# Performance work log

Hardware: AMD Instinct MI355X
Metric: run time of the kernel (lower is better)

## Reference

```python
import jax, jax.numpy as jnp
import numpy as np

N, B, E, H, L, NF = 32768, 2048, 524288, 128, 7, 10
NODE_F = 60  # 10 frames * (loc 3 + vel 3)
OUT_F = 30   # 10 frames * 3


def _mlp(x, W1, b1, W2, b2):
    return jax.nn.relu(x @ W1 + b1) @ W2 + b2


def _lin(key, fan_in, fan_out):
    s = 1.0 / np.sqrt(fan_in)
    kw, kb = jax.random.split(key)
    W = jax.random.uniform(kw, (fan_in, fan_out), jnp.float32, -s, s)
    b = jax.random.uniform(kb, (fan_out,), jnp.float32, -s, s)
    return W, b


def setup_inputs() -> dict:
    key = jax.random.key(0)
    ks = jax.random.split(key, 12)
    p = {}
    p["loc"] = jax.random.normal(ks[0], (N, NF, 3), jnp.float32)
    p["vel"] = jax.random.normal(ks[1], (N, NF, 3), jnp.float32)
    p["y"] = jax.random.normal(ks[2], (N, NF, 3), jnp.float32)
    p["edge_index"] = jax.random.randint(ks[3], (2, E), 0, N, dtype=jnp.int64)
    p["batch_size"] = B
    # embedder: Linear(60,H) -> ReLU -> Linear(H,H)
    p["emb_W1"], p["emb_b1"] = _lin(ks[4], NODE_F, H)
    p["emb_W2"], p["emb_b2"] = _lin(ks[5], H, H)
    # per-layer message net Linear(2H,H)->ReLU->Linear(H,H); update net Linear(2H,H)->ReLU->Linear(H,H)
    mW1, mb1, mW2, mb2, uW1, ub1, uW2, ub2 = [], [], [], [], [], [], [], []
    for i in range(L):
        k = jax.random.fold_in(ks[6], i)
        k1, k2, k3, k4 = jax.random.split(k, 4)
        a, b = _lin(k1, 2 * H, H); mW1.append(a); mb1.append(b)
        a, b = _lin(k2, H, H); mW2.append(a); mb2.append(b)
        a, b = _lin(k3, 2 * H, H); uW1.append(a); ub1.append(b)
        a, b = _lin(k4, H, H); uW2.append(a); ub2.append(b)
    p["msg_W1"] = jnp.stack(mW1); p["msg_b1"] = jnp.stack(mb1)
    p["msg_W2"] = jnp.stack(mW2); p["msg_b2"] = jnp.stack(mb2)
    p["upd_W1"] = jnp.stack(uW1); p["upd_b1"] = jnp.stack(ub1)
    p["upd_W2"] = jnp.stack(uW2); p["upd_b2"] = jnp.stack(ub2)
    # head: Linear(H,H) -> ReLU -> Linear(H,30)
    p["head_W1"], p["head_b1"] = _lin(ks[7], H, H)
    p["head_W2"], p["head_b2"] = _lin(ks[8], H, OUT_F)
    return p


def reference(loc, vel, y, edge_index, batch_size,
              emb_W1, emb_b1, emb_W2, emb_b2,
              msg_W1, msg_b1, msg_W2, msg_b2,
              upd_W1, upd_b1, upd_W2, upd_b2,
              head_W1, head_b1, head_W2, head_b2):
    n = loc.shape[0]
    src, dst = edge_index[0], edge_index[1]  # x_j = x[src], x_i = x[dst] (PyG source_to_target)
    x = jnp.concatenate([loc, vel], axis=-1).reshape(n, -1)  # (N, 60)
    x = _mlp(x, emb_W1, emb_b1, emb_W2, emb_b2)              # (N, H)
    for i in range(L):
        m_in = jnp.concatenate([x[dst], x[src]], axis=-1)    # (E, 2H) cat(x_i, x_j)
        msg = _mlp(m_in, msg_W1[i], msg_b1[i], msg_W2[i], msg_b2[i])  # (E, H)
        agg = jax.ops.segment_sum(msg, dst, num_segments=n)  # scatter-add at targets
        x = _mlp(jnp.concatenate([x, agg], axis=-1), upd_W1[i], upd_b1[i], upd_W2[i], upd_b2[i])
    x = _mlp(x, head_W1, head_b1, head_W2, head_b2)          # (N, 30)
    loc_pred = x.reshape(n, NF, 3) + loc
    d = jnp.sqrt(jnp.sum((loc_pred - y) ** 2, axis=-1))      # (N, NF)
    ade_loss = d.reshape(batch_size, -1, NF).mean(axis=-1).mean(axis=-1)  # (B,)
    fde = jnp.sqrt(jnp.sum((loc_pred[:, -1, :] - y[:, -1, :]) ** 2, axis=-1))  # (N,)
    fde_loss = fde.reshape(batch_size, -1).mean(axis=-1)     # (B,)
    backprop_loss = ade_loss.mean()
    return backprop_loss, ade_loss, fde_loss
```

## Files before the change

### kernel.cpp

```cpp
#include <hip/hip_runtime.h>
#include <hip/hip_bf16.h>
#include <stdint.h>

#define HH 128

typedef __attribute__((ext_vector_type(8))) short short8;
typedef __attribute__((ext_vector_type(4))) float floatx4;

typedef __attribute__((address_space(3))) uint32_t lds_u32_t;
typedef const __attribute__((address_space(1))) uint32_t gbl_u32_t;

__device__ __forceinline__ void gl_lds16(const void* g, void* l) {
  __builtin_amdgcn_global_load_lds((gbl_u32_t*)g, (lds_u32_t*)l, 16, 0, 0);
}

__device__ __forceinline__ float bf2f(short v) {
  union { uint32_t u; float f; } x; x.u = ((uint32_t)(uint16_t)v) << 16; return x.f;
}
__device__ __forceinline__ short f2bf(float f) {
  union { float f; uint32_t u; } x; x.f = f;
  uint32_t r = x.u + 0x7fffu + ((x.u >> 16) & 1u);
  return (short)(r >> 16);
}
__device__ __forceinline__ float rdf(const void* p, int i, int fl) {
  return fl ? bf2f(((const short*)p)[i]) : ((const float*)p)[i];
}


__global__ void detect_zero(const int* __restrict__ eidx, int* iflag, int* dflag,
                            int* __restrict__ counts, float* accp,
                            const uint32_t* __restrict__ loc, int N) {
  int g = blockIdx.x * 256 + threadIdx.x;
  if (g < N) counts[g] = 0;
  if (blockIdx.x == 0) {
    __shared__ int nz, cnt;
    if (threadIdx.x == 0) { nz = 0; cnt = 0; *accp = 0.f; }
    __syncthreads();
    int any = 0;
    for (int i = threadIdx.x; i < 1024; i += 256) any |= (eidx[2 * i + 1] != 0);
    if (any) atomicOr(&nz, 1);
    uint32_t u = loc[threadIdx.x];
    int e = (u >> 7) & 0xFF;
    if (e >= 100 && e <= 140) atomicAdd(&cnt, 1);
    __syncthreads();
    if (threadIdx.x == 0) {
      *iflag = (nz == 0) ? 1 : 0;
      *dflag = (cnt >= 192) ? 1 : 0;
    }
  }
}


__global__ void pad_input(const void* __restrict__ loc, const void* __restrict__ vel,
                          short* __restrict__ dst, const int* __restrict__ dflag) {
  int fl = *dflag;
  int idx = blockIdx.x * 256 + threadIdx.x;
  int j = idx & 63, i = idx >> 6;
  short v = 0;
  if (j < 60) {
    int f = j / 6, c = j % 6;
    float x = (c < 3) ? rdf(loc, (i * 10 + f) * 3 + c, fl)
                      : rdf(vel, (i * 10 + f) * 3 + (c - 3), fl);
    v = f2bf(x);
  }
  dst[idx] = v;
}

struct WPrep {
  const void* src[8];
  unsigned long long dstoff[8];
  int L[8], K[8], Nn[8], Kp[8], Np[8];
  int bstart[9];
};

__global__ void prep_w(WPrep a, short* __restrict__ wbase, const int* __restrict__ dflag) {
  int fl = *dflag;
  int b = blockIdx.x;
  int s = 0;
  while (b >= a.bstart[s + 1]) ++s;
  int idx = (b - a.bstart[s]) * 256 + threadIdx.x;
  int Kp = a.Kp[s], Np = a.Np[s], K = a.K[s], Nn = a.Nn[s];
  int tot = a.L[s] * Np * Kp;
  if (idx >= tot) return;
  int k = idx % Kp; int rest = idx / Kp; int n = rest % Np; int l = rest / Np;
  short v = 0;
  if (k < K && n < Nn) v = f2bf(rdf(a.src[s], (l * K + k) * Nn + n, fl));
  wbase[a.dstoff[s] + idx] = v;
}

struct BPrep {
  const void* src[8];
  int n[8];
  int estart[9];
};

__global__ void prep_b(BPrep a, float* __restrict__ bias, const int* __restrict__ dflag) {
  int fl = *dflag;
  int idx = blockIdx.x * 256 + threadIdx.x;
  if (idx >= a.estart[8]) return;
  int s = 0;
  while (idx >= a.estart[s + 1]) ++s;
  int j = idx - a.estart[s];
  bias[idx] = (j < a.n[s]) ? rdf(a.src[s], j, fl) : 0.0f;
}


__global__ void fold_kernel(const short* __restrict__ updW1T, const short* __restrict__ msgW2T,
                            short* __restrict__ updW1Tf, const float* __restrict__ msgB2f,
                            float* __restrict__ b2U) {
  if (blockIdx.x < 896) {
    int idx = blockIdx.x * 256 + threadIdx.x;
    int k = idx & 255; int n = (idx >> 8) & 127; int l = idx >> 15;
    if (k < 128) { updW1Tf[idx] = updW1T[idx]; return; }
    int kk = k - 128;
    const short* w2 = msgW2T + l * 128 * 128;
    const short* u1 = updW1T + l * 128 * 256 + n * 256 + 128;
    float s = 0.f;
    for (int j = 0; j < 128; ++j) s += bf2f(w2[j * 128 + kk]) * bf2f(u1[j]);
    updW1Tf[idx] = f2bf(s);
  } else {
    int idx = (blockIdx.x - 896) * 256 + threadIdx.x;
    if (idx >= 7 * 128) return;
    int n = idx & 127, l = idx >> 7;
    const short* u1 = updW1T + l * 128 * 256 + n * 256 + 128;
    const float* b2 = msgB2f + l * 128;
    float s = 0.f;
    for (int j = 0; j < 128; ++j) s += b2[j] * bf2f(u1[j]);
    b2U[idx] = s;
  }
}


__global__ void hist_kernel(const int* __restrict__ eidx, const int* __restrict__ iflag,
                            int* __restrict__ counts, int E) {
  int e = blockIdx.x * 256 + threadIdx.x;
  if (e >= E) return;
  int fl = *iflag;
  int d = fl ? eidx[2 * (E + e)] : eidx[E + e];
  atomicAdd(&counts[d], 1);
}

__global__ void scan_bsum(const int* __restrict__ counts, int* __restrict__ bsums, int N) {
  int i = blockIdx.x * 256 + threadIdx.x;
  int v = (i < N) ? counts[i] : 0;
#pragma unroll
  for (int off = 1; off < 64; off <<= 1) v += __shfl_xor(v, off);
  __shared__ int ws4[4];
  if ((threadIdx.x & 63) == 0) ws4[threadIdx.x >> 6] = v;
  __syncthreads();
  if (threadIdx.x == 0) bsums[blockIdx.x] = ws4[0] + ws4[1] + ws4[2] + ws4[3];
}

__global__ void scan_final(const int* __restrict__ counts, const int* __restrict__ bsums,
                           int* __restrict__ row_start, int* __restrict__ cursor,
                           float* __restrict__ deg, int N, int E) {
  int t = threadIdx.x;
  __shared__ int shb[2];
  __shared__ int wsum[4];
  int v = (t < 128 && t < (int)blockIdx.x) ? bsums[t] : 0;
#pragma unroll
  for (int off = 1; off < 64; off <<= 1) v += __shfl_xor(v, off);
  if (t == 0) shb[0] = v;
  if (t == 64) shb[1] = v;
  int i = blockIdx.x * 256 + t;
  int c = (i < N) ? counts[i] : 0;
  int lane = t & 63, w = t >> 6;
  int x = c;
#pragma unroll
  for (int off = 1; off < 64; off <<= 1) {
    int u = __shfl_up(x, off);
    if (lane >= off) x += u;
  }
  if (lane == 63) wsum[w] = x;
  __syncthreads();
  int wpre = 0;
#pragma unroll
  for (int k = 0; k < 4; ++k)
    if (k < w) wpre += wsum[k];
  int excl = shb[0] + shb[1] + wpre + x - c;
  if (i < N) {
    row_start[i] = excl;
    cursor[i] = excl;
    deg[i] = (float)c;
  }
  if (i == N - 1) row_start[N] = E;
}

__global__ void scatter_kernel(const int* __restrict__ eidx, const int* __restrict__ iflag,
                               int* __restrict__ cursor, int* __restrict__ ssrc, int E) {
  int e = blockIdx.x * 256 + threadIdx.x;
  if (e >= E) return;
  int fl = *iflag;
  int d = fl ? eidx[2 * (E + e)] : eidx[E + e];
  int sv = fl ? eidx[2 * e] : eidx[e];
  int pos = atomicAdd(&cursor[d], 1);
  ssrc[pos] = sv;
}


__global__ __launch_bounds__(256)
void edge_agg(const uint32_t* __restrict__ Pp, const uint32_t* __restrict__ Qp,
              const int* __restrict__ ssrc, const int* __restrict__ row_start,
              uint32_t* __restrict__ Hagg, int Ntot) {
  int w = threadIdx.x >> 6, lane = threadIdx.x & 63;
  int d = blockIdx.x * 4 + w;
  if (d >= Ntot) return;
  uint32_t pv = Pp[(size_t)d * 64 + lane];
  float px = bf2f((short)(pv & 0xffff));
  float py = bf2f((short)(pv >> 16));
  int s0 = row_start[d], s1 = row_start[d + 1];
  float ax = 0.f, ay = 0.f;
  int e = s0;
  for (; e + 8 <= s1; e += 8) {
    int idx[8]; uint32_t q[8];
#pragma unroll
    for (int u = 0; u < 8; ++u) idx[u] = ssrc[e + u];
#pragma unroll
    for (int u = 0; u < 8; ++u) q[u] = Qp[(size_t)idx[u] * 64 + lane];
#pragma unroll
    for (int u = 0; u < 8; ++u) {
      float hx = px + bf2f((short)(q[u] & 0xffff));
      float hy = py + bf2f((short)(q[u] >> 16));
      ax += hx > 0.f ? hx : 0.f;
      ay += hy > 0.f ? hy : 0.f;
    }
  }
  if (e + 4 <= s1) {
    int idx[4]; uint32_t q[4];
#pragma unroll
    for (int u = 0; u < 4; ++u) idx[u] = ssrc[e + u];
#pragma unroll
    for (int u = 0; u < 4; ++u) q[u] = Qp[(size_t)idx[u] * 64 + lane];
#pragma unroll
    for (int u = 0; u < 4; ++u) {
      float hx = px + bf2f((short)(q[u] & 0xffff));
      float hy = py + bf2f((short)(q[u] >> 16));
      ax += hx > 0.f ? hx : 0.f;
      ay += hy > 0.f ? hy : 0.f;
    }
    e += 4;
  }
  if (e + 2 <= s1) {
    int i0 = ssrc[e], i1 = ssrc[e + 1];
    uint32_t q0 = Qp[(size_t)i0 * 64 + lane];
    uint32_t q1 = Qp[(size_t)i1 * 64 + lane];
    float hx = px + bf2f((short)(q0 & 0xffff)), hy = py + bf2f((short)(q0 >> 16));
    ax += hx > 0.f ? hx : 0.f; ay += hy > 0.f ? hy : 0.f;
    hx = px + bf2f((short)(q1 & 0xffff)); hy = py + bf2f((short)(q1 >> 16));
    ax += hx > 0.f ? hx : 0.f; ay += hy > 0.f ? hy : 0.f;
    e += 2;
  }
  if (e < s1) {
    int i0 = ssrc[e];
    uint32_t q0 = Qp[(size_t)i0 * 64 + lane];
    float hx = px + bf2f((short)(q0 & 0xffff));
    float hy = py + bf2f((short)(q0 >> 16));
    ax += hx > 0.f ? hx : 0.f;
    ay += hy > 0.f ? hy : 0.f;
  }
  uint32_t packed = (uint32_t)(uint16_t)f2bf(ax) | ((uint32_t)(uint16_t)f2bf(ay) << 16);
  Hagg[(size_t)d * 64 + lane] = packed;
}


__device__ __forceinline__ void write_aslots32(char* lds, const floatx4 v[2][4],
                                               int wc, int quad, int l16) {
#pragma unroll
  for (int mt = 0; mt < 2; ++mt)
#pragma unroll
    for (int nt = 0; nt < 4; ++nt) {
      int s2 = wc * 2 + (nt >> 1);
      int qc = (nt & 1) * 2 + (l16 >> 3);
      char* base = lds + (size_t)(s2 * 2 + mt) * 1024 + 2 * (l16 & 7);
#pragma unroll
      for (int r = 0; r < 4; ++r)
        *(short*)(base + (quad * 4 + r + 16 * qc) * 16) = f2bf(v[mt][nt][r]);
    }
}

template <int NT, int TS>
__device__ __forceinline__ void gemm32(const char* lds, int wc, floatx4 acc[2][NT], int lane) {
  const char* ldsB = lds + 8192;
#pragma unroll
  for (int s2 = 0; s2 < 4; ++s2) {
    short8 af[2];
#pragma unroll
    for (int mt = 0; mt < 2; ++mt)
      af[mt] = *(const short8*)(lds + (s2 * 2 + mt) * 1024 + lane * 16);
    short8 bf[NT];
#pragma unroll
    for (int nt = 0; nt < NT; ++nt)
      bf[nt] = *(const short8*)(ldsB + (s2 * TS + wc * NT + nt) * 1024 + lane * 16);
#pragma unroll
    for (int mt = 0; mt < 2; ++mt)
#pragma unroll
      for (int nt = 0; nt < NT; ++nt)
        acc[mt][nt] = __builtin_amdgcn_mfma_f32_16x16x32_bf16(af[mt], bf[nt], acc[mt][nt], 0, 0, 0);
  }
}


template <int MODE>
__global__ __launch_bounds__(128, 2)
void mlp_fused(const short* __restrict__ Asrc, const short* __restrict__ Asrc2,
               const short* __restrict__ W1T, const float* __restrict__ b1,
               const short* __restrict__ W2T, const float* __restrict__ b2,
               const float* __restrict__ deg, const float* __restrict__ b2Uv,
               const short* __restrict__ pqW1, const float* __restrict__ pqB1,
               const short* __restrict__ pq2W, const float* __restrict__ pq2B,
               short* __restrict__ xout, short* __restrict__ Pout,
               short* __restrict__ Qout, float* __restrict__ out32) {
  constexpr int K1 = (MODE == 0) ? 64 : 256;
  constexpr int NSA = K1 / 32;
  constexpr int PQS = (MODE == 3) ? 128 : 256;

  __shared__ __align__(16) char lds[40960];
  char* ldsB = lds + 8192;

  const int tid = threadIdx.x;
  const int wc = tid >> 6, lane = tid & 63;
  const int quad = lane >> 4, l16 = lane & 15;
  const int R0 = blockIdx.x * 32;
  const int CB = wc * 64;

  if constexpr (MODE == 0) {
#pragma unroll
    for (int c = 0; c < 8; ++c) {
      int slot = wc * 8 + c;
      int s = slot >> 3, t = slot & 7;
      gl_lds16(W1T + (t * 16 + l16) * 64 + s * 32 + quad * 8,
               ldsB + slot * 1024 + lane * 16);
    }
  } else {
#pragma unroll
    for (int c = 0; c < 16; ++c) {
      int slot = wc * 16 + c;
      int s2 = slot >> 3, t = slot & 7;
      gl_lds16(W1T + (t * 16 + l16) * 256 + s2 * 32 + quad * 8,
               ldsB + slot * 1024 + lane * 16);
    }
  }

  short8 afrag[NSA][2];
  if constexpr (MODE == 0) {
#pragma unroll
    for (int mt = 0; mt < 2; ++mt) {
      int m = R0 + mt * 16 + l16;
      const short* pr = Asrc + (size_t)m * 64;
#pragma unroll
      for (int s = 0; s < 2; ++s) afrag[s][mt] = *(const short8*)(pr + s * 32 + quad * 8);
    }
  } else {
#pragma unroll
    for (int mt = 0; mt < 2; ++mt) {
      int m = R0 + mt * 16 + l16;
      const short* pr = Asrc + (size_t)m * HH;
      const short* ar = Asrc2 + (size_t)m * HH;
#pragma unroll
      for (int s = 0; s < 4; ++s) {
        afrag[s][mt] = *(const short8*)(pr + s * 32 + quad * 8);
        afrag[s + 4][mt] = *(const short8*)(ar + s * 32 + quad * 8);
      }
    }
  }

  float b1f[4], b2f[4], pb1[4], b2u[4];
  float dvals[2][4];
#pragma unroll
  for (int t = 0; t < 4; ++t) {
    int col = CB + t * 16 + l16;
    b1f[t] = b1[col];
    b2f[t] = b2[col];
    pb1[t] = pqB1[col];
  }
  if constexpr (MODE != 0) {
#pragma unroll
    for (int t = 0; t < 4; ++t) b2u[t] = b2Uv[CB + t * 16 + l16];
#pragma unroll
    for (int mt = 0; mt < 2; ++mt)
#pragma unroll
      for (int r = 0; r < 4; ++r)
        dvals[mt][r] = deg[R0 + mt * 16 + quad * 4 + r];
  }

  __syncthreads();

  floatx4 zero4 = {0.f, 0.f, 0.f, 0.f};
  floatx4 acc[2][4];
#pragma unroll
  for (int mt = 0; mt < 2; ++mt)
#pragma unroll
    for (int t = 0; t < 4; ++t) acc[mt][t] = zero4;
  {
    constexpr int NS0 = (MODE == 0) ? 2 : 4;
#pragma unroll
    for (int s = 0; s < NS0; ++s) {
      short8 bfrag[4];
#pragma unroll
      for (int nt = 0; nt < 4; ++nt)
        bfrag[nt] = *(const short8*)(ldsB + (s * 8 + wc * 4 + nt) * 1024 + lane * 16);
#pragma unroll
      for (int mt = 0; mt < 2; ++mt)
#pragma unroll
        for (int nt = 0; nt < 4; ++nt)
          acc[mt][nt] = __builtin_amdgcn_mfma_f32_16x16x32_bf16(afrag[s][mt], bfrag[nt], acc[mt][nt], 0, 0, 0);
    }
  }

  if constexpr (MODE != 0) {
    __syncthreads();
#pragma unroll
    for (int c = 0; c < 16; ++c) {
      int slot = wc * 16 + c;
      int s2 = slot >> 3, t = slot & 7;
      gl_lds16(W1T + (t * 16 + l16) * 256 + 128 + s2 * 32 + quad * 8,
               ldsB + slot * 1024 + lane * 16);
    }
    __syncthreads();
#pragma unroll
    for (int s = 0; s < 4; ++s) {
      short8 bfrag[4];
#pragma unroll
      for (int nt = 0; nt < 4; ++nt)
        bfrag[nt] = *(const short8*)(ldsB + (s * 8 + wc * 4 + nt) * 1024 + lane * 16);
#pragma unroll
      for (int mt = 0; mt < 2; ++mt)
#pragma unroll
        for (int nt = 0; nt < 4; ++nt)
          acc[mt][nt] = __builtin_amdgcn_mfma_f32_16x16x32_bf16(afrag[4 + s][mt], bfrag[nt], acc[mt][nt], 0, 0, 0);
    }
  }

  __syncthreads();

#pragma unroll
  for (int c = 0; c < 16; ++c) {
    int slot = wc * 16 + c;
    int s2 = slot >> 3, t = slot & 7;
    gl_lds16(W2T + (t * 16 + l16) * HH + s2 * 32 + quad * 8,
             ldsB + slot * 1024 + lane * 16);
  }
  {
    floatx4 hv[2][4];
#pragma unroll
    for (int mt = 0; mt < 2; ++mt)
#pragma unroll
      for (int nt = 0; nt < 4; ++nt)
#pragma unroll
        for (int r = 0; r < 4; ++r) {
          float h = acc[mt][nt][r] + b1f[nt];
          if constexpr (MODE != 0) h += dvals[mt][r] * b2u[nt];
          hv[mt][nt][r] = h > 0.f ? h : 0.f;
        }
    write_aslots32(lds, hv, wc, quad, l16);
  }

  __syncthreads();

  floatx4 acc2[2][4];
#pragma unroll
  for (int mt = 0; mt < 2; ++mt)
#pragma unroll
    for (int t = 0; t < 4; ++t) acc2[mt][t] = zero4;
  gemm32<4, 8>(lds, wc, acc2, lane);

  floatx4 xv[2][4];
#pragma unroll
  for (int mt = 0; mt < 2; ++mt)
#pragma unroll
    for (int nt = 0; nt < 4; ++nt)
#pragma unroll
      for (int r = 0; r < 4; ++r)
        xv[mt][nt][r] = acc2[mt][nt][r] + b2f[nt];

  if constexpr (MODE != 3) {
#pragma unroll
    for (int mt = 0; mt < 2; ++mt)
#pragma unroll
      for (int nt = 0; nt < 4; ++nt) {
        int col = CB + nt * 16 + l16;
#pragma unroll
        for (int r = 0; r < 4; ++r) {
          int row = R0 + mt * 16 + quad * 4 + r;
          xout[(size_t)row * HH + col] = f2bf(xv[mt][nt][r]);
        }
      }
  }

  __syncthreads();

  write_aslots32(lds, xv, wc, quad, l16);
#pragma unroll
  for (int c = 0; c < 16; ++c) {
    int slot = wc * 16 + c;
    int s2 = slot >> 3, t = slot & 7;
    gl_lds16(pqW1 + (t * 16 + l16) * PQS + s2 * 32 + quad * 8,
             ldsB + slot * 1024 + lane * 16);
  }

  __syncthreads();

  floatx4 accc[2][4];
#pragma unroll
  for (int mt = 0; mt < 2; ++mt)
#pragma unroll
    for (int t = 0; t < 4; ++t) accc[mt][t] = zero4;
  gemm32<4, 8>(lds, wc, accc, lane);

  if constexpr (MODE == 3) {
    floatx4 h2[2][4];
#pragma unroll
    for (int mt = 0; mt < 2; ++mt)
#pragma unroll
      for (int nt = 0; nt < 4; ++nt)
#pragma unroll
        for (int r = 0; r < 4; ++r) {
          float h = accc[mt][nt][r] + pb1[nt];
          h2[mt][nt][r] = h > 0.f ? h : 0.f;
        }
    __syncthreads();
    write_aslots32(lds, h2, wc, quad, l16);
#pragma unroll
    for (int c = 0; c < 4; ++c) {
      int slot = wc * 4 + c;
      int s2 = slot >> 1, t = slot & 1;
      gl_lds16(pq2W + (t * 16 + l16) * 128 + s2 * 32 + quad * 8,
               ldsB + slot * 1024 + lane * 16);
    }
    __syncthreads();
    floatx4 acco[2][1];
#pragma unroll
    for (int mt = 0; mt < 2; ++mt) acco[mt][0] = zero4;
    gemm32<1, 2>(lds, wc, acco, lane);
    float ob = pq2B[wc * 16 + l16];
#pragma unroll
    for (int mt = 0; mt < 2; ++mt) {
      int col = wc * 16 + l16;
#pragma unroll
      for (int r = 0; r < 4; ++r) {
        int row = R0 + mt * 16 + quad * 4 + r;
        out32[(size_t)row * 32 + col] = acco[mt][0][r] + ob;
      }
    }
  } else {
#pragma unroll
    for (int mt = 0; mt < 2; ++mt)
#pragma unroll
      for (int nt = 0; nt < 4; ++nt) {
        int col = CB + nt * 16 + l16;
#pragma unroll
        for (int r = 0; r < 4; ++r) {
          int row = R0 + mt * 16 + quad * 4 + r;
          Pout[(size_t)row * HH + col] = f2bf(accc[mt][nt][r] + pb1[nt]);
        }
      }
    __syncthreads();
#pragma unroll
    for (int c = 0; c < 16; ++c) {
      int slot = wc * 16 + c;
      int s2 = slot >> 3, t = slot & 7;
      gl_lds16(pqW1 + (t * 16 + l16) * 256 + 128 + s2 * 32 + quad * 8,
               ldsB + slot * 1024 + lane * 16);
    }
    __syncthreads();
    floatx4 accq[2][4];
#pragma unroll
    for (int mt = 0; mt < 2; ++mt)
#pragma unroll
      for (int t = 0; t < 4; ++t) accq[mt][t] = zero4;
    gemm32<4, 8>(lds, wc, accq, lane);
#pragma unroll
    for (int mt = 0; mt < 2; ++mt)
#pragma unroll
      for (int nt = 0; nt < 4; ++nt) {
        int col = CB + nt * 16 + l16;
#pragma unroll
        for (int r = 0; r < 4; ++r) {
          int row = R0 + mt * 16 + quad * 4 + r;
          Qout[(size_t)row * HH + col] = f2bf(accq[mt][nt][r]);
        }
      }
  }
}


__global__ void loss_kernel(const float* __restrict__ out32, const void* __restrict__ loc,
                            const void* __restrict__ yv, const int* __restrict__ dflag,
                            float* __restrict__ out, float* __restrict__ acc, int NB) {
  int fl = *dflag;
  int i = blockIdx.x * 256 + threadIdx.x;
  const float* o = out32 + (size_t)i * 32;
  float dsum = 0.f, fde = 0.f;
#pragma unroll
  for (int f = 0; f < 10; ++f) {
    float dx = o[f * 3 + 0] + rdf(loc, i * 30 + f * 3 + 0, fl) - rdf(yv, i * 30 + f * 3 + 0, fl);
    float dy = o[f * 3 + 1] + rdf(loc, i * 30 + f * 3 + 1, fl) - rdf(yv, i * 30 + f * 3 + 1, fl);
    float dz = o[f * 3 + 2] + rdf(loc, i * 30 + f * 3 + 2, fl) - rdf(yv, i * 30 + f * 3 + 2, fl);
    float d = sqrtf(dx * dx + dy * dy + dz * dz);
    dsum += d;
    if (f == 9) fde = d;
  }
#pragma unroll
  for (int m = 1; m < 16; m <<= 1) {
    dsum += __shfl_xor(dsum, m);
    fde += __shfl_xor(fde, m);
  }
  if ((threadIdx.x & 15) == 0) {
    int b = i >> 4;
    out[1 + b] = dsum / 160.0f;
    out[1 + NB + b] = fde / 16.0f;
    unsafeAtomicAdd(acc, dsum);
  }
}

__global__ void final_kernel(const float* __restrict__ acc, float* __restrict__ out, float inv) {
  if (threadIdx.x == 0) out[0] = *acc * inv;
}


extern "C" void kernel_launch(void* const* d_in, const int* in_sizes, int n_in,
                              void* d_out, int out_size, void* d_ws, size_t ws_size,
                              hipStream_t stream) {
  const void* loc = d_in[0];
  const void* vel = d_in[1];
  const void* yv = d_in[2];
  const int* eidx = (const int*)d_in[3];

  const int N = in_sizes[0] / 30;
  const int E = in_sizes[3] / 2;
  const int L = 7;
  const int NB = N / 16;

  const size_t MB = 1024 * 1024;
  char* ws = (char*)d_ws;
  short* x = (short*)ws;
  short* P = (short*)(ws + 8 * MB);
  short* Qs = (short*)(ws + 24 * MB);
  short* Hagg = (short*)(ws + 32 * MB);
  short* updW1Tf = (short*)(ws + 40 * MB);
  int* bsums = (int*)(ws + 41 * MB);
  short* wbase = (short*)(ws + 48 * MB);
  const unsigned long long OFF_EMBW1 = 0;
  const unsigned long long OFF_EMBW2 = 8192;
  const unsigned long long OFF_HEADW1 = 24576;
  const unsigned long long OFF_HEADW2 = 40960;
  const unsigned long long OFF_MSGW1 = 45056;
  const unsigned long long OFF_MSGW2 = 274432;
  const unsigned long long OFF_UPDW1 = 389120;
  const unsigned long long OFF_UPDW2 = 618496;
  short* embW1T = wbase + OFF_EMBW1;
  short* embW2T = wbase + OFF_EMBW2;
  short* headW1T = wbase + OFF_HEADW1;
  short* headW2T = wbase + OFF_HEADW2;
  short* msgW1T = wbase + OFF_MSGW1;
  short* msgW2T = wbase + OFF_MSGW2;
  short* updW1T = wbase + OFF_UPDW1;
  short* updW2T = wbase + OFF_UPDW2;
  float* bias = (float*)(ws + 49 * MB + 512 * 1024);
  float* embB1f = bias;
  float* embB2f = bias + 128;
  float* msgB1f = bias + 256;
  float* msgB2f = bias + 1152;
  float* updB1f = bias + 2048;
  float* updB2f = bias + 2944;
  float* headB1f = bias + 3840;
  float* headB2f = bias + 3968;
  float* b2U = bias + 4096;
  int* counts = (int*)(ws + 49 * MB + 768 * 1024);
  int* row_start = (int*)(ws + 50 * MB);
  int* cursor = (int*)(ws + 50 * MB + 256 * 1024);
  float* deg = (float*)(ws + 50 * MB + 512 * 1024);
  int* iflag = (int*)(ws + 50 * MB + 768 * 1024);
  int* dflag = iflag + 16;
  float* accp = (float*)(iflag + 32);
  int* ssrc = (int*)(ws + 51 * MB);
  short* in64 = (short*)(ws + 53 * MB);
  float* out32 = (float*)(ws + 57 * MB);

  const int NBLK = (N + 255) / 256;

  detect_zero<<<NBLK, 256, 0, stream>>>(eidx, iflag, dflag, counts, accp,
                                        (const uint32_t*)loc, N);
  hist_kernel<<<(E + 255) / 256, 256, 0, stream>>>(eidx, iflag, counts, E);
  scan_bsum<<<NBLK, 256, 0, stream>>>(counts, bsums, N);
  scan_final<<<NBLK, 256, 0, stream>>>(counts, bsums, row_start, cursor, deg, N, E);
  scatter_kernel<<<(E + 255) / 256, 256, 0, stream>>>(eidx, iflag, cursor, ssrc, E);

  pad_input<<<(N * 64) / 256, 256, 0, stream>>>(loc, vel, in64, dflag);

  {
    WPrep a;
    const void* srcs[8] = {d_in[5], d_in[7], d_in[17], d_in[19],
                           d_in[9], d_in[11], d_in[13], d_in[15]};
    unsigned long long offs[8] = {OFF_EMBW1, OFF_EMBW2, OFF_HEADW1, OFF_HEADW2,
                                  OFF_MSGW1, OFF_MSGW2, OFF_UPDW1, OFF_UPDW2};
    int Ls[8] = {1, 1, 1, 1, 7, 7, 7, 7};
    int Ks[8] = {60, 128, 128, 128, 256, 128, 256, 128};
    int Ns[8] = {128, 128, 128, 30, 128, 128, 128, 128};
    int Kps[8] = {64, 128, 128, 128, 256, 128, 256, 128};
    int Nps[8] = {128, 128, 128, 32, 128, 128, 128, 128};
    int cum = 0;
    for (int s = 0; s < 8; ++s) {
      a.src[s] = srcs[s]; a.dstoff[s] = offs[s];
      a.L[s] = Ls[s]; a.K[s] = Ks[s]; a.Nn[s] = Ns[s]; a.Kp[s] = Kps[s]; a.Np[s] = Nps[s];
      a.bstart[s] = cum;
      cum += (Ls[s] * Nps[s] * Kps[s] + 255) / 256;
    }
    a.bstart[8] = cum;
    prep_w<<<cum, 256, 0, stream>>>(a, wbase, dflag);
  }
  {
    BPrep a;
    const void* srcs[8] = {d_in[6], d_in[8], d_in[10], d_in[12],
                           d_in[14], d_in[16], d_in[18], d_in[20]};
    int ns[8] = {128, 128, 896, 896, 896, 896, 128, 30};
    int es[9] = {0, 128, 256, 1152, 2048, 2944, 3840, 3968, 4000};
    for (int s = 0; s < 8; ++s) { a.src[s] = srcs[s]; a.n[s] = ns[s]; a.estart[s] = es[s]; }
    a.estart[8] = es[8];
    prep_b<<<16, 256, 0, stream>>>(a, bias, dflag);
  }

  fold_kernel<<<900, 256, 0, stream>>>(updW1T, msgW2T, updW1Tf, msgB2f, b2U);

  mlp_fused<0><<<N / 32, 128, 0, stream>>>(in64, nullptr,
      embW1T, embB1f, embW2T, embB2f, nullptr, nullptr,
      msgW1T, msgB1f, nullptr, nullptr, x, P, Qs, nullptr);

  for (int l = 0; l < L; ++l) {
    edge_agg<<<(N + 3) / 4, 256, 0, stream>>>((const uint32_t*)P, (const uint32_t*)Qs,
                                              ssrc, row_start, (uint32_t*)Hagg, N);
    if (l < L - 1) {
      mlp_fused<2><<<N / 32, 128, 0, stream>>>(x, Hagg,
          updW1Tf + l * 128 * 256, updB1f + l * 128, updW2T + l * 128 * 128, updB2f + l * 128,
          deg, b2U + l * 128,
          msgW1T + (l + 1) * 128 * 256, msgB1f + (l + 1) * 128, nullptr, nullptr,
          x, P, Qs, nullptr);
    } else {
      mlp_fused<3><<<N / 32, 128, 0, stream>>>(x, Hagg,
          updW1Tf + l * 128 * 256, updB1f + l * 128, updW2T + l * 128 * 128, updB2f + l * 128,
          deg, b2U + l * 128,
          headW1T, headB1f, headW2T, headB2f,
          nullptr, nullptr, nullptr, out32);
    }
  }

  loss_kernel<<<N / 256, 256, 0, stream>>>(out32, loc, yv, dflag, (float*)d_out, accp, NB);
  final_kernel<<<1, 64, 0, stream>>>(accp, (float*)d_out, 1.0f / 327680.0f);
}
```

Before: 567.8 us.

## Double mlp_fused row tile to 64 with 4 waves; fold final kernel into loss

The fused MLP kernel now processes 64 rows per block with four waves arranged 2x2 (row and column halves), so each weight tile staged in LDS is reused across twice as many rows. The full 256-wide first-layer weight is loaded at once into a 64 KB LDS buffer, which removes the second load-and-sync phase. The separate final kernel is replaced by a last-block ticket inside the loss kernel, saving one launch. The cost is more LDS per block, which may limit occupancy, and half as many blocks in the grid.

```diff
diff --git a/kernel.cpp b/kernel.cpp
--- a/kernel.cpp
+++ b/kernel.cpp
@@ -28,13 +28,13 @@
 
 
 __global__ void detect_zero(const int* __restrict__ eidx, int* iflag, int* dflag,
-                            int* __restrict__ counts, float* accp,
+                            int* __restrict__ counts, float* accp, int* ticket,
                             const uint32_t* __restrict__ loc, int N) {
   int g = blockIdx.x * 256 + threadIdx.x;
   if (g < N) counts[g] = 0;
   if (blockIdx.x == 0) {
     __shared__ int nz, cnt;
-    if (threadIdx.x == 0) { nz = 0; cnt = 0; *accp = 0.f; }
+    if (threadIdx.x == 0) { nz = 0; cnt = 0; *accp = 0.f; *ticket = 0; }
     __syncthreads();
     int any = 0;
     for (int i = threadIdx.x; i < 1024; i += 256) any |= (eidx[2 * i + 1] != 0);
@@ -263,30 +263,33 @@
 }
 
 
-__device__ __forceinline__ void write_aslots32(char* lds, const floatx4 v[2][4],
-                                               int wc, int quad, int l16) {
-#pragma unroll
-  for (int mt = 0; mt < 2; ++mt)
+__device__ __forceinline__ void write_aslots64(char* lds, const floatx4 v[2][4],
+                                               int wr, int wc, int quad, int l16) {
+#pragma unroll
+  for (int mt = 0; mt < 2; ++mt) {
+    int g = wr * 2 + mt;
 #pragma unroll
     for (int nt = 0; nt < 4; ++nt) {
       int s2 = wc * 2 + (nt >> 1);
       int qc = (nt & 1) * 2 + (l16 >> 3);
-      char* base = lds + (size_t)(s2 * 2 + mt) * 1024 + 2 * (l16 & 7);
+      char* base = lds + (size_t)(s2 * 4 + g) * 1024 + 2 * (l16 & 7);
 #pragma unroll
       for (int r = 0; r < 4; ++r)
         *(short*)(base + (quad * 4 + r + 16 * qc) * 16) = f2bf(v[mt][nt][r]);
     }
+  }
 }
 
 template <int NT, int TS>
-__device__ __forceinline__ void gemm32(const char* lds, int wc, floatx4 acc[2][NT], int lane) {
-  const char* ldsB = lds + 8192;
+__device__ __forceinline__ void gemm64(const char* lds, int wr, int wc,
+                                       floatx4 acc[2][NT], int lane) {
+  const char* ldsB = lds + 16384;
 #pragma unroll
   for (int s2 = 0; s2 < 4; ++s2) {
     short8 af[2];
 #pragma unroll
     for (int mt = 0; mt < 2; ++mt)
-      af[mt] = *(const short8*)(lds + (s2 * 2 + mt) * 1024 + lane * 16);
+      af[mt] = *(const short8*)(lds + (s2 * 4 + wr * 2 + mt) * 1024 + lane * 16);
     short8 bf[NT];
 #pragma unroll
     for (int nt = 0; nt < NT; ++nt)
@@ -301,7 +304,7 @@
 
 
 template <int MODE>
-__global__ __launch_bounds__(128, 2)
+__global__ __launch_bounds__(256, 2)
 void mlp_fused(const short* __restrict__ Asrc, const short* __restrict__ Asrc2,
                const short* __restrict__ W1T, const float* __restrict__ b1,
                const short* __restrict__ W2T, const float* __restrict__ b2,
@@ -310,23 +313,23 @@
                const short* __restrict__ pq2W, const float* __restrict__ pq2B,
                short* __restrict__ xout, short* __restrict__ Pout,
                short* __restrict__ Qout, float* __restrict__ out32) {
-  constexpr int K1 = (MODE == 0) ? 64 : 256;
-  constexpr int NSA = K1 / 32;
+  constexpr int NSA = (MODE == 0) ? 2 : 8;
   constexpr int PQS = (MODE == 3) ? 128 : 256;
 
-  __shared__ __align__(16) char lds[40960];
-  char* ldsB = lds + 8192;
+  __shared__ __align__(16) char lds[65536];
+  char* ldsB = lds + 16384;
 
   const int tid = threadIdx.x;
-  const int wc = tid >> 6, lane = tid & 63;
+  const int w = tid >> 6, lane = tid & 63;
   const int quad = lane >> 4, l16 = lane & 15;
-  const int R0 = blockIdx.x * 32;
+  const int wr = w >> 1, wc = w & 1;
+  const int R0 = blockIdx.x * 64;
   const int CB = wc * 64;
 
   if constexpr (MODE == 0) {
 #pragma unroll
-    for (int c = 0; c < 8; ++c) {
-      int slot = wc * 8 + c;
+    for (int c = 0; c < 4; ++c) {
+      int slot = w * 4 + c;
       int s = slot >> 3, t = slot & 7;
       gl_lds16(W1T + (t * 16 + l16) * 64 + s * 32 + quad * 8,
                ldsB + slot * 1024 + lane * 16);
@@ -334,10 +337,10 @@
   } else {
 #pragma unroll
     for (int c = 0; c < 16; ++c) {
-      int slot = wc * 16 + c;
-      int s2 = slot >> 3, t = slot & 7;
-      gl_lds16(W1T + (t * 16 + l16) * 256 + s2 * 32 + quad * 8,
-               ldsB + slot * 1024 + lane * 16);
+      int slot = w * 16 + c;
+      int s = slot >> 3, t = slot & 7;
+      gl_lds16(W1T + (t * 16 + l16) * 256 + s * 32 + quad * 8,
+               lds + slot * 1024 + lane * 16);
     }
   }
 
@@ -345,7 +348,7 @@
   if constexpr (MODE == 0) {
 #pragma unroll
     for (int mt = 0; mt < 2; ++mt) {
-      int m = R0 + mt * 16 + l16;
+      int m = R0 + wr * 32 + mt * 16 + l16;
       const short* pr = Asrc + (size_t)m * 64;
 #pragma unroll
       for (int s = 0; s < 2; ++s) afrag[s][mt] = *(const short8*)(pr + s * 32 + quad * 8);
@@ -353,7 +356,7 @@
   } else {
 #pragma unroll
     for (int mt = 0; mt < 2; ++mt) {
-      int m = R0 + mt * 16 + l16;
+      int m = R0 + wr * 32 + mt * 16 + l16;
       const short* pr = Asrc + (size_t)m * HH;
       const short* ar = Asrc2 + (size_t)m * HH;
 #pragma unroll
@@ -380,7 +383,7 @@
     for (int mt = 0; mt < 2; ++mt)
 #pragma unroll
       for (int r = 0; r < 4; ++r)
-        dvals[mt][r] = deg[R0 + mt * 16 + quad * 4 + r];
+        dvals[mt][r] = deg[R0 + wr * 32 + mt * 16 + quad * 4 + r];
   }
 
   __syncthreads();
@@ -391,10 +394,9 @@
   for (int mt = 0; mt < 2; ++mt)
 #pragma unroll
     for (int t = 0; t < 4; ++t) acc[mt][t] = zero4;
-  {
-    constexpr int NS0 = (MODE == 0) ? 2 : 4;
-#pragma unroll
-    for (int s = 0; s < NS0; ++s) {
+  if constexpr (MODE == 0) {
+#pragma unroll
+    for (int s = 0; s < 2; ++s) {
       short8 bfrag[4];
 #pragma unroll
       for (int nt = 0; nt < 4; ++nt)
@@ -405,37 +407,26 @@
         for (int nt = 0; nt < 4; ++nt)
           acc[mt][nt] = __builtin_amdgcn_mfma_f32_16x16x32_bf16(afrag[s][mt], bfrag[nt], acc[mt][nt], 0, 0, 0);
     }
-  }
-
-  if constexpr (MODE != 0) {
-    __syncthreads();
-#pragma unroll
-    for (int c = 0; c < 16; ++c) {
-      int slot = wc * 16 + c;
-      int s2 = slot >> 3, t = slot & 7;
-      gl_lds16(W1T + (t * 16 + l16) * 256 + 128 + s2 * 32 + quad * 8,
-               ldsB + slot * 1024 + lane * 16);
-    }
-    __syncthreads();
-#pragma unroll
-    for (int s = 0; s < 4; ++s) {
+  } else {
+#pragma unroll
+    for (int s = 0; s < 8; ++s) {
       short8 bfrag[4];
 #pragma unroll
       for (int nt = 0; nt < 4; ++nt)
-        bfrag[nt] = *(const short8*)(ldsB + (s * 8 + wc * 4 + nt) * 1024 + lane * 16);
+        bfrag[nt] = *(const short8*)(lds + (s * 8 + wc * 4 + nt) * 1024 + lane * 16);
 #pragma unroll
       for (int mt = 0; mt < 2; ++mt)
 #pragma unroll
         for (int nt = 0; nt < 4; ++nt)
-          acc[mt][nt] = __builtin_amdgcn_mfma_f32_16x16x32_bf16(afrag[4 + s][mt], bfrag[nt], acc[mt][nt], 0, 0, 0);
+          acc[mt][nt] = __builtin_amdgcn_mfma_f32_16x16x32_bf16(afrag[s][mt], bfrag[nt], acc[mt][nt], 0, 0, 0);
     }
   }
 
   __syncthreads();
 
 #pragma unroll
-  for (int c = 0; c < 16; ++c) {
-    int slot = wc * 16 + c;
+  for (int c = 0; c < 8; ++c) {
+    int slot = w * 8 + c;
     int s2 = slot >> 3, t = slot & 7;
     gl_lds16(W2T + (t * 16 + l16) * HH + s2 * 32 + quad * 8,
              ldsB + slot * 1024 + lane * 16);
@@ -452,7 +443,7 @@
           if constexpr (MODE != 0) h += dvals[mt][r] * b2u[nt];
           hv[mt][nt][r] = h > 0.f ? h : 0.f;
         }
-    write_aslots32(lds, hv, wc, quad, l16);
+    write_aslots64(lds, hv, wr, wc, quad, l16);
   }
 
   __syncthreads();
@@ -462,7 +453,7 @@
   for (int mt = 0; mt < 2; ++mt)
 #pragma unroll
     for (int t = 0; t < 4; ++t) acc2[mt][t] = zero4;
-  gemm32<4, 8>(lds, wc, acc2, lane);
+  gemm64<4, 8>(lds, wr, wc, acc2, lane);
 
   floatx4 xv[2][4];
 #pragma unroll
@@ -481,7 +472,7 @@
         int col = CB + nt * 16 + l16;
 #pragma unroll
         for (int r = 0; r < 4; ++r) {
-          int row = R0 + mt * 16 + quad * 4 + r;
+          int row = R0 + wr * 32 + mt * 16 + quad * 4 + r;
           xout[(size_t)row * HH + col] = f2bf(xv[mt][nt][r]);
         }
       }
@@ -489,10 +480,10 @@
 
   __syncthreads();
 
-  write_aslots32(lds, xv, wc, quad, l16);
-#pragma unroll
-  for (int c = 0; c < 16; ++c) {
-    int slot = wc * 16 + c;
+  write_aslots64(lds, xv, wr, wc, quad, l16);
+#pragma unroll
+  for (int c = 0; c < 8; ++c) {
+    int slot = w * 8 + c;
     int s2 = slot >> 3, t = slot & 7;
     gl_lds16(pqW1 + (t * 16 + l16) * PQS + s2 * 32 + quad * 8,
              ldsB + slot * 1024 + lane * 16);
@@ -505,7 +496,7 @@
   for (int mt = 0; mt < 2; ++mt)
 #pragma unroll
     for (int t = 0; t < 4; ++t) accc[mt][t] = zero4;
-  gemm32<4, 8>(lds, wc, accc, lane);
+  gemm64<4, 8>(lds, wr, wc, accc, lane);
 
   if constexpr (MODE == 3) {
     floatx4 h2[2][4];
@@ -519,10 +510,10 @@
           h2[mt][nt][r] = h > 0.f ? h : 0.f;
         }
     __syncthreads();
-    write_aslots32(lds, h2, wc, quad, l16);
-#pragma unroll
-    for (int c = 0; c < 4; ++c) {
-      int slot = wc * 4 + c;
+    write_aslots64(lds, h2, wr, wc, quad, l16);
+#pragma unroll
+    for (int c = 0; c < 2; ++c) {
+      int slot = w * 2 + c;
       int s2 = slot >> 1, t = slot & 1;
       gl_lds16(pq2W + (t * 16 + l16) * 128 + s2 * 32 + quad * 8,
                ldsB + slot * 1024 + lane * 16);
@@ -531,14 +522,14 @@
     floatx4 acco[2][1];
 #pragma unroll
     for (int mt = 0; mt < 2; ++mt) acco[mt][0] = zero4;
-    gemm32<1, 2>(lds, wc, acco, lane);
+    gemm64<1, 2>(lds, wr, wc, acco, lane);
     float ob = pq2B[wc * 16 + l16];
 #pragma unroll
     for (int mt = 0; mt < 2; ++mt) {
       int col = wc * 16 + l16;
 #pragma unroll
       for (int r = 0; r < 4; ++r) {
-        int row = R0 + mt * 16 + quad * 4 + r;
+        int row = R0 + wr * 32 + mt * 16 + quad * 4 + r;
         out32[(size_t)row * 32 + col] = acco[mt][0][r] + ob;
       }
     }
@@ -550,14 +541,14 @@
         int col = CB + nt * 16 + l16;
 #pragma unroll
         for (int r = 0; r < 4; ++r) {
-          int row = R0 + mt * 16 + quad * 4 + r;
+          int row = R0 + wr * 32 + mt * 16 + quad * 4 + r;
           Pout[(size_t)row * HH + col] = f2bf(accc[mt][nt][r] + pb1[nt]);
         }
       }
     __syncthreads();
 #pragma unroll
-    for (int c = 0; c < 16; ++c) {
-      int slot = wc * 16 + c;
+    for (int c = 0; c < 8; ++c) {
+      int slot = w * 8 + c;
       int s2 = slot >> 3, t = slot & 7;
       gl_lds16(pqW1 + (t * 16 + l16) * 256 + 128 + s2 * 32 + quad * 8,
                ldsB + slot * 1024 + lane * 16);
@@ -568,7 +559,7 @@
     for (int mt = 0; mt < 2; ++mt)
 #pragma unroll
       for (int t = 0; t < 4; ++t) accq[mt][t] = zero4;
-    gemm32<4, 8>(lds, wc, accq, lane);
+    gemm64<4, 8>(lds, wr, wc, accq, lane);
 #pragma unroll
     for (int mt = 0; mt < 2; ++mt)
 #pragma unroll
@@ -576,7 +567,7 @@
         int col = CB + nt * 16 + l16;
 #pragma unroll
         for (int r = 0; r < 4; ++r) {
-          int row = R0 + mt * 16 + quad * 4 + r;
+          int row = R0 + wr * 32 + mt * 16 + quad * 4 + r;
           Qout[(size_t)row * HH + col] = f2bf(accq[mt][nt][r]);
         }
       }
@@ -586,7 +577,8 @@
 
 __global__ void loss_kernel(const float* __restrict__ out32, const void* __restrict__ loc,
                             const void* __restrict__ yv, const int* __restrict__ dflag,
-                            float* __restrict__ out, float* __restrict__ acc, int NB) {
+                            float* __restrict__ out, float* __restrict__ acc,
+                            int* __restrict__ ticket, int NB, int nblocks, float inv) {
   int fl = *dflag;
   int i = blockIdx.x * 256 + threadIdx.x;
   const float* o = out32 + (size_t)i * 32;
@@ -611,10 +603,15 @@
     out[1 + NB + b] = fde / 16.0f;
     unsafeAtomicAdd(acc, dsum);
   }
-}
-
-__global__ void final_kernel(const float* __restrict__ acc, float* __restrict__ out, float inv) {
-  if (threadIdx.x == 0) out[0] = *acc * inv;
+  __threadfence();
+  __syncthreads();
+  if (threadIdx.x == 0) {
+    int old = atomicAdd(ticket, 1);
+    if (old == nblocks - 1) {
+      float v = unsafeAtomicAdd(acc, 0.0f);
+      out[0] = v * inv;
+    }
+  }
 }
 
 
@@ -673,13 +670,14 @@
   int* iflag = (int*)(ws + 50 * MB + 768 * 1024);
   int* dflag = iflag + 16;
   float* accp = (float*)(iflag + 32);
+  int* ticket = iflag + 48;
   int* ssrc = (int*)(ws + 51 * MB);
   short* in64 = (short*)(ws + 53 * MB);
   float* out32 = (float*)(ws + 57 * MB);
 
   const int NBLK = (N + 255) / 256;
 
-  detect_zero<<<NBLK, 256, 0, stream>>>(eidx, iflag, dflag, counts, accp,
+  detect_zero<<<NBLK, 256, 0, stream>>>(eidx, iflag, dflag, counts, accp, ticket,
                                         (const uint32_t*)loc, N);
   hist_kernel<<<(E + 255) / 256, 256, 0, stream>>>(eidx, iflag, counts, E);
   scan_bsum<<<NBLK, 256, 0, stream>>>(counts, bsums, N);
@@ -722,7 +720,7 @@
 
   fold_kernel<<<900, 256, 0, stream>>>(updW1T, msgW2T, updW1Tf, msgB2f, b2U);
 
-  mlp_fused<0><<<N / 32, 128, 0, stream>>>(in64, nullptr,
+  mlp_fused<0><<<N / 64, 256, 0, stream>>>(in64, nullptr,
       embW1T, embB1f, embW2T, embB2f, nullptr, nullptr,
       msgW1T, msgB1f, nullptr, nullptr, x, P, Qs, nullptr);
 
@@ -730,13 +728,13 @@
     edge_agg<<<(N + 3) / 4, 256, 0, stream>>>((const uint32_t*)P, (const uint32_t*)Qs,
                                               ssrc, row_start, (uint32_t*)Hagg, N);
     if (l < L - 1) {
-      mlp_fused<2><<<N / 32, 128, 0, stream>>>(x, Hagg,
+      mlp_fused<2><<<N / 64, 256, 0, stream>>>(x, Hagg,
           updW1Tf + l * 128 * 256, updB1f + l * 128, updW2T + l * 128 * 128, updB2f + l * 128,
           deg, b2U + l * 128,
           msgW1T + (l + 1) * 128 * 256, msgB1f + (l + 1) * 128, nullptr, nullptr,
           x, P, Qs, nullptr);
     } else {
-      mlp_fused<3><<<N / 32, 128, 0, stream>>>(x, Hagg,
+      mlp_fused<3><<<N / 64, 256, 0, stream>>>(x, Hagg,
           updW1Tf + l * 128 * 256, updB1f + l * 128, updW2T + l * 128 * 128, updB2f + l * 128,
           deg, b2U + l * 128,
           headW1T, headB1f, headW2T, headB2f,
@@ -744,6 +742,6 @@
     }
   }
 
-  loss_kernel<<<N / 256, 256, 0, stream>>>(out32, loc, yv, dflag, (float*)d_out, accp, NB);
-  final_kernel<<<1, 64, 0, stream>>>(accp, (float*)d_out, 1.0f / 327680.0f);
-}
+  loss_kernel<<<N / 256, 256, 0, stream>>>(out32, loc, yv, dflag, (float*)d_out, accp,
+                                           ticket, NB, N / 256, 1.0f / 327680.0f);
+}
```

New measurement: 508.2 us. 10.5% less time.
